# Optimization experiments

Hardware: AMD Instinct MI355X
Metric: run time of the kernel (lower is better)

## Reference

```python
import jax, jax.numpy as jnp
import numpy as np

N = 4096        # n_nodes; must equal HID due to the model's mean(dim=1)->classifier quirk
IN_DIM = 512
HID = 4096
E = 65536       # N * avg_degree(16)


def _lin(k, out_dim, in_dim):
    return jax.random.normal(k, (out_dim, in_dim), jnp.float32) * 0.02


def setup_inputs() -> dict:
    key = jax.random.key(0)
    ks = jax.random.split(key, 8)
    return {
        "x": jax.random.normal(ks[0], (N, IN_DIM), jnp.float32),
        "edge_index": jax.random.randint(ks[1], (2, E), 0, N, dtype=jnp.int32),
        "W_embed": _lin(ks[2], HID, IN_DIM),
        "b_embed": jnp.zeros((HID,), jnp.float32),
        "W1": _lin(ks[3], HID, HID),
        "b1": jnp.zeros((HID,), jnp.float32),
        "W2": _lin(ks[4], HID, HID),
        "b2": jnp.zeros((HID,), jnp.float32),
        "Wc1": _lin(ks[5], HID // 2, HID),
        "bc1": jnp.zeros((HID // 2,), jnp.float32),
        "Wc2": _lin(ks[6], 1, HID // 2),
        "bc2": jnp.zeros((1,), jnp.float32),
    }


def reference(x, edge_index, W_embed, b_embed, W1, b1, W2, b2, Wc1, bc1, Wc2, bc2):
    row, col = edge_index[0], edge_index[1]
    # embed: Linear(in_dim, hidden)
    h = x @ W_embed.T + b_embed                       # [N, HID]
    # two GNN layers: gather neighbors, scatter-add, linear + relu
    for W, b in ((W1, b1), (W2, b2)):
        aggr = jax.ops.segment_sum(h[col], row, num_segments=h.shape[0])  # [N, HID]
        h = jax.nn.relu(aggr @ W.T + b)
    # faithful to original: mean over feature dim -> [N] (N == HID)
    hm = jnp.mean(h, axis=1)                          # [HID]
    z = jax.nn.relu(hm @ Wc1.T + bc1)                 # [HID//2]
    out = (z @ Wc2.T + bc2).squeeze(-1)               # scalar
    return out
```

## Files before the change

### kernel.cpp

```cpp
#include <hip/hip_runtime.h>
#include <hip/hip_bf16.h>


#define N_NODES 4096
#define IN_DIM_ 512
#define HID_ 4096
#define NEDGE 65536

typedef float f32x4 __attribute__((ext_vector_type(4)));
typedef float f32x2 __attribute__((ext_vector_type(2)));
typedef unsigned short u16x8 __attribute__((ext_vector_type(8)));
typedef int i32x8 __attribute__((ext_vector_type(8)));

#define ACT_SCALE 8.0f
#define W_SCALE 256.0f
#define G_SCALE 8.0f
#define G_STORE_MUL (8.0f / 2048.0f)

__device__ __forceinline__ unsigned short f2bf(float f) {
  unsigned u = __float_as_uint(f);
  return (unsigned short)((u + 0x7fffu + ((u >> 16) & 1u)) >> 16);
}
__device__ __forceinline__ float bf2f(unsigned short h) {
  return __uint_as_float((unsigned)h << 16);
}
__device__ __forceinline__ unsigned char f2fp8(float f) {
  int w = __builtin_amdgcn_cvt_pk_fp8_f32(f, f, 0, false);
  return (unsigned char)(w & 0xff);
}
__device__ __forceinline__ void fp8x4_acc(int w, float* acc) {
  f32x2 lo = __builtin_amdgcn_cvt_pk_f32_fp8(w, false);
  f32x2 hi = __builtin_amdgcn_cvt_pk_f32_fp8(w, true);
  acc[0] += lo[0]; acc[1] += lo[1]; acc[2] += hi[0]; acc[3] += hi[1];
}

__global__ __launch_bounds__(256) void cvt_fp8(const float* __restrict__ in,
                                               unsigned char* __restrict__ out,
                                               int n, float scale) {
  int i = (blockIdx.x * 256 + threadIdx.x) * 8;
  if (i >= n) return;
  const float4 a = *(const float4*)(in + i);
  const float4 b = *(const float4*)(in + i + 4);
  int w0 = __builtin_amdgcn_cvt_pk_fp8_f32(a.x * scale, a.y * scale, 0, false);
  w0 = __builtin_amdgcn_cvt_pk_fp8_f32(a.z * scale, a.w * scale, w0, true);
  int w1 = __builtin_amdgcn_cvt_pk_fp8_f32(b.x * scale, b.y * scale, 0, false);
  w1 = __builtin_amdgcn_cvt_pk_fp8_f32(b.z * scale, b.w * scale, w1, true);
  *(int2*)(out + i) = make_int2(w0, w1);
}

__global__ __launch_bounds__(256) void zero_i32(int* __restrict__ p, int n) {
  int i = blockIdx.x * 256 + threadIdx.x;
  if (i < n) p[i] = 0;
}

__global__ __launch_bounds__(256) void hist_rows(const int* __restrict__ row,
                                                 int* __restrict__ counts) {
  int e = blockIdx.x * 256 + threadIdx.x;
  if (e < NEDGE) atomicAdd(&counts[row[e]], 1);
}

__global__ __launch_bounds__(1024) void scan4096(const int* __restrict__ counts,
                                                 int* __restrict__ starts) {
  __shared__ int sa[1024], sb[1024];
  const int t = threadIdx.x;
  const int c0 = counts[t * 4], c1 = counts[t * 4 + 1],
            c2 = counts[t * 4 + 2], c3 = counts[t * 4 + 3];
  const int local = c0 + c1 + c2 + c3;
  sa[t] = local;
  __syncthreads();
  int* src = sa; int* dst = sb;
  for (int off = 1; off < 1024; off <<= 1) {
    int v = src[t];
    if (t >= off) v += src[t - off];
    dst[t] = v;
    __syncthreads();
    int* tmp = src; src = dst; dst = tmp;
  }
  const int excl = (t == 0) ? 0 : src[t - 1];
  starts[t * 4]     = excl;
  starts[t * 4 + 1] = excl + c0;
  starts[t * 4 + 2] = excl + c0 + c1;
  starts[t * 4 + 3] = excl + c0 + c1 + c2;
  if (t == 1023) starts[4096] = excl + local;
}

__global__ __launch_bounds__(256) void fill_adj(const int* __restrict__ row,
                                                const int* __restrict__ col,
                                                const int* __restrict__ starts,
                                                int* __restrict__ cursor,
                                                int* __restrict__ adj) {
  int e = blockIdx.x * 256 + threadIdx.x;
  if (e >= NEDGE) return;
  int r = row[e];
  int p = atomicAdd(&cursor[r], 1);
  adj[starts[r] + p] = col[e];
}

__device__ __forceinline__ i32x8 ld_frag(const char* base0) {
  const int4 lo = *(const int4*)(base0);
  const int4 hi = *(const int4*)(base0 + 8192);
  i32x8 f;
  f[0] = lo.x; f[1] = lo.y; f[2] = lo.z; f[3] = lo.w;
  f[4] = hi.x; f[5] = hi.y; f[6] = hi.z; f[7] = hi.w;
  return f;
}

__global__ __launch_bounds__(256) void gemm_mx(
    const unsigned char* __restrict__ A, const unsigned char* __restrict__ B,
    unsigned char* __restrict__ C, int N, int K,
    const float* __restrict__ bias, float mul) {
  __shared__ unsigned char As[128 * 128];
  __shared__ unsigned char Bs[128 * 128];
  const int t = threadIdx.x;
  const int bm = blockIdx.x * 128, bn = blockIdx.y * 128;
  const int wave = t >> 6, lane = t & 63;
  const int wm = (wave >> 1) * 64, wn = (wave & 1) * 64;
  const int m16 = lane & 15, quad = lane >> 4;

  f32x4 acc[4][4] = {};

  const int srow = t >> 2;
  const int sg = (t & 3) * 32;
  const unsigned char* Ag0 = A + (size_t)(bm + srow) * K + sg;
  const unsigned char* Ag1 = A + (size_t)(bm + 64 + srow) * K + sg;
  const unsigned char* Bg0 = B + (size_t)(bn + srow) * K + sg;
  const unsigned char* Bg1 = B + (size_t)(bn + 64 + srow) * K + sg;
  char* AsB = (char*)As;
  char* BsB = (char*)Bs;

#define GLDS(gp, lp)                                                       \
  __builtin_amdgcn_global_load_lds(                                        \
      (const __attribute__((address_space(1))) void*)(gp),                 \
      (__attribute__((address_space(3))) void*)(lp), 16, 0, 0)

  for (int kb = 0; kb < K; kb += 128) {
    GLDS(Ag0 + kb,      AsB + t * 16);
    GLDS(Ag1 + kb,      AsB + 4096 + t * 16);
    GLDS(Ag0 + kb + 16, AsB + 8192 + t * 16);
    GLDS(Ag1 + kb + 16, AsB + 12288 + t * 16);
    GLDS(Bg0 + kb,      BsB + t * 16);
    GLDS(Bg1 + kb,      BsB + 4096 + t * 16);
    GLDS(Bg0 + kb + 16, BsB + 8192 + t * 16);
    GLDS(Bg1 + kb + 16, BsB + 12288 + t * 16);
    __syncthreads();

    i32x8 af[4], bfr[4];
#pragma unroll
    for (int r = 0; r < 4; ++r)
      af[r] = ld_frag(AsB + (wm + r * 16 + m16) * 64 + quad * 16);
#pragma unroll
    for (int c = 0; c < 4; ++c)
      bfr[c] = ld_frag(BsB + (wn + c * 16 + m16) * 64 + quad * 16);
#pragma unroll
    for (int r = 0; r < 4; ++r)
#pragma unroll
      for (int c = 0; c < 4; ++c)
        acc[r][c] = __builtin_amdgcn_mfma_scale_f32_16x16x128_f8f6f4(
            af[r], bfr[c], acc[r][c], 0, 0,
            0, 0x7f7f7f7f, 0, 0x7f7f7f7f);
    __syncthreads();
  }
#undef GLDS

#pragma unroll
  for (int r = 0; r < 4; ++r) {
#pragma unroll
    for (int c = 0; c < 4; ++c) {
      const int row0 = bm + wm + r * 16 + quad * 4;
      const int col = bn + wn + c * 16 + m16;
      const float bv = bias ? ACT_SCALE * bias[col] : 0.0f;
#pragma unroll
      for (int i = 0; i < 4; ++i) {
        C[(size_t)(row0 + i) * N + col] = f2fp8(acc[r][c][i] * mul + bv);
      }
    }
  }
}

__global__ __launch_bounds__(256) void aggr_f8out(
    const unsigned char* __restrict__ g, const int* __restrict__ starts,
    const int* __restrict__ adj, const float* __restrict__ bias,
    unsigned char* __restrict__ hout) {
  const int node = blockIdx.y;
  const int f0 = blockIdx.x * 2048 + threadIdx.x * 8;
  float acc[8] = {0, 0, 0, 0, 0, 0, 0, 0};
  const int s = starts[node], e = starts[node + 1];
  int j = s;
  for (; j + 4 <= e; j += 4) {
    const int c0 = adj[j], c1 = adj[j + 1], c2 = adj[j + 2], c3 = adj[j + 3];
    int2 v0 = *(const int2*)(g + (size_t)c0 * HID_ + f0);
    int2 v1 = *(const int2*)(g + (size_t)c1 * HID_ + f0);
    int2 v2 = *(const int2*)(g + (size_t)c2 * HID_ + f0);
    int2 v3 = *(const int2*)(g + (size_t)c3 * HID_ + f0);
    fp8x4_acc(v0.x, acc);     fp8x4_acc(v0.y, acc + 4);
    fp8x4_acc(v1.x, acc);     fp8x4_acc(v1.y, acc + 4);
    fp8x4_acc(v2.x, acc);     fp8x4_acc(v2.y, acc + 4);
    fp8x4_acc(v3.x, acc);     fp8x4_acc(v3.y, acc + 4);
  }
  for (; j < e; ++j) {
    int2 v = *(const int2*)(g + (size_t)adj[j] * HID_ + f0);
    fp8x4_acc(v.x, acc);      fp8x4_acc(v.y, acc + 4);
  }
  const float4 b0 = *(const float4*)(bias + f0);
  const float4 b1 = *(const float4*)(bias + f0 + 4);
  const float bb[8] = {b0.x, b0.y, b0.z, b0.w, b1.x, b1.y, b1.z, b1.w};
  float v[8];
#pragma unroll
  for (int i = 0; i < 8; ++i)
    v[i] = ACT_SCALE * fmaxf(acc[i] * (1.0f / G_SCALE) + bb[i], 0.0f);
  int w0 = __builtin_amdgcn_cvt_pk_fp8_f32(v[0], v[1], 0, false);
  w0 = __builtin_amdgcn_cvt_pk_fp8_f32(v[2], v[3], w0, true);
  int w1 = __builtin_amdgcn_cvt_pk_fp8_f32(v[4], v[5], 0, false);
  w1 = __builtin_amdgcn_cvt_pk_fp8_f32(v[6], v[7], w1, true);
  *(int2*)(hout + (size_t)node * HID_ + f0) = make_int2(w0, w1);
}

__global__ __launch_bounds__(256) void aggr_bf16out(
    const unsigned char* __restrict__ g, const int* __restrict__ starts,
    const int* __restrict__ adj, const float* __restrict__ bias,
    unsigned short* __restrict__ hout) {
  const int node = blockIdx.y;
  const int f0 = blockIdx.x * 2048 + threadIdx.x * 8;
  float acc[8] = {0, 0, 0, 0, 0, 0, 0, 0};
  const int s = starts[node], e = starts[node + 1];
  int j = s;
  for (; j + 4 <= e; j += 4) {
    const int c0 = adj[j], c1 = adj[j + 1], c2 = adj[j + 2], c3 = adj[j + 3];
    int2 v0 = *(const int2*)(g + (size_t)c0 * HID_ + f0);
    int2 v1 = *(const int2*)(g + (size_t)c1 * HID_ + f0);
    int2 v2 = *(const int2*)(g + (size_t)c2 * HID_ + f0);
    int2 v3 = *(const int2*)(g + (size_t)c3 * HID_ + f0);
    fp8x4_acc(v0.x, acc);     fp8x4_acc(v0.y, acc + 4);
    fp8x4_acc(v1.x, acc);     fp8x4_acc(v1.y, acc + 4);
    fp8x4_acc(v2.x, acc);     fp8x4_acc(v2.y, acc + 4);
    fp8x4_acc(v3.x, acc);     fp8x4_acc(v3.y, acc + 4);
  }
  for (; j < e; ++j) {
    int2 v = *(const int2*)(g + (size_t)adj[j] * HID_ + f0);
    fp8x4_acc(v.x, acc);      fp8x4_acc(v.y, acc + 4);
  }
  const float4 b0 = *(const float4*)(bias + f0);
  const float4 b1 = *(const float4*)(bias + f0 + 4);
  const float bb[8] = {b0.x, b0.y, b0.z, b0.w, b1.x, b1.y, b1.z, b1.w};
  u16x8 r;
#pragma unroll
  for (int i = 0; i < 8; ++i)
    r[i] = f2bf(fmaxf(acc[i] * (1.0f / G_SCALE) + bb[i], 0.0f));
  *(u16x8*)(hout + (size_t)node * HID_ + f0) = r;
}

__global__ __launch_bounds__(256) void row_mean(const unsigned short* __restrict__ h,
                                                float* __restrict__ hm) {
  const int row = blockIdx.x, t = threadIdx.x;
  const u16x8* p = (const u16x8*)(h + (size_t)row * HID_);
  u16x8 v1 = p[t], v2 = p[t + 256];
  float s = 0.f;
#pragma unroll
  for (int i = 0; i < 8; ++i) s += bf2f(v1[i]) + bf2f(v2[i]);
  for (int off = 32; off > 0; off >>= 1) s += __shfl_down(s, off);
  __shared__ float ws[4];
  if ((t & 63) == 0) ws[t >> 6] = s;
  __syncthreads();
  if (t == 0) hm[row] = (ws[0] + ws[1] + ws[2] + ws[3]) * (1.0f / (float)HID_);
}

__global__ __launch_bounds__(256) void clf1(const float* __restrict__ Wc1,
                                            const float* __restrict__ bc1,
                                            const float* __restrict__ hm,
                                            float* __restrict__ z) {
  const int wave = threadIdx.x >> 6, lane = threadIdx.x & 63;
  const int j = blockIdx.x * 4 + wave;
  const float* w = Wc1 + (size_t)j * HID_;
  float s = 0.f;
  for (int i = lane; i < HID_; i += 64) s += w[i] * hm[i];
  for (int off = 32; off > 0; off >>= 1) s += __shfl_down(s, off);
  if (lane == 0) z[j] = fmaxf(s + bc1[j], 0.0f);
}

__global__ __launch_bounds__(256) void clf2(const float* __restrict__ Wc2,
                                            const float* __restrict__ bc2,
                                            const float* __restrict__ z,
                                            float* __restrict__ out) {
  const int t = threadIdx.x;
  float s = 0.f;
  for (int i = t; i < HID_ / 2; i += 256) s += z[i] * Wc2[i];
  for (int off = 32; off > 0; off >>= 1) s += __shfl_down(s, off);
  __shared__ float ws[4];
  if ((t & 63) == 0) ws[t >> 6] = s;
  __syncthreads();
  if (t == 0) out[0] = ws[0] + ws[1] + ws[2] + ws[3] + bc2[0];
}

extern "C" void kernel_launch(void* const* d_in, const int* in_sizes, int n_in,
                              void* d_out, int out_size, void* d_ws, size_t ws_size,
                              hipStream_t stream) {
  (void)in_sizes; (void)n_in; (void)out_size; (void)ws_size;
  const float* x       = (const float*)d_in[0];
  const int*   edge    = (const int*)d_in[1];
  const int*   row     = edge;
  const int*   col     = edge + NEDGE;
  const float* W_embed = (const float*)d_in[2];
  const float* b_embed = (const float*)d_in[3];
  const float* W1      = (const float*)d_in[4];
  const float* b1      = (const float*)d_in[5];
  const float* W2      = (const float*)d_in[6];
  const float* b2      = (const float*)d_in[7];
  const float* Wc1     = (const float*)d_in[8];
  const float* bc1     = (const float*)d_in[9];
  const float* Wc2     = (const float*)d_in[10];
  const float* bc2     = (const float*)d_in[11];
  float* out = (float*)d_out;

  char* ws = (char*)d_ws;
  size_t off = 0;
  auto alloc = [&](size_t bytes) {
    char* p = ws + off;
    off += (bytes + 255) & ~(size_t)255;
    return p;
  };
  unsigned char*  xf8  = (unsigned char*)alloc((size_t)N_NODES * IN_DIM_);
  unsigned char*  wef8 = (unsigned char*)alloc((size_t)HID_ * IN_DIM_);
  unsigned char*  w1f8 = (unsigned char*)alloc((size_t)HID_ * HID_);
  unsigned char*  w2f8 = (unsigned char*)alloc((size_t)HID_ * HID_);
  unsigned char*  h0f8 = (unsigned char*)alloc((size_t)N_NODES * HID_);
  unsigned char*  h1f8 = (unsigned char*)alloc((size_t)N_NODES * HID_);
  unsigned char*  g    = (unsigned char*)alloc((size_t)N_NODES * HID_);
  unsigned short* h2   = (unsigned short*)alloc((size_t)N_NODES * HID_ * 2);
  int* counts = (int*)alloc(N_NODES * 4);
  int* cursor = (int*)alloc(N_NODES * 4);
  int* starts = (int*)alloc((N_NODES + 1) * 4);
  int* adj    = (int*)alloc(NEDGE * 4);
  float* hm   = (float*)alloc(N_NODES * 4);
  float* z    = (float*)alloc((HID_ / 2) * 4);

  zero_i32<<<16, 256, 0, stream>>>(counts, N_NODES);
  zero_i32<<<16, 256, 0, stream>>>(cursor, N_NODES);
  hist_rows<<<NEDGE / 256, 256, 0, stream>>>(row, counts);
  scan4096<<<1, 1024, 0, stream>>>(counts, starts);
  fill_adj<<<NEDGE / 256, 256, 0, stream>>>(row, col, starts, cursor, adj);

  cvt_fp8<<<(N_NODES * IN_DIM_ / 8) / 256, 256, 0, stream>>>(x, xf8, N_NODES * IN_DIM_, ACT_SCALE);
  cvt_fp8<<<(HID_ * IN_DIM_ / 8) / 256, 256, 0, stream>>>(W_embed, wef8, HID_ * IN_DIM_, W_SCALE);
  cvt_fp8<<<(HID_ * HID_ / 8) / 256, 256, 0, stream>>>(W1, w1f8, HID_ * HID_, W_SCALE);
  cvt_fp8<<<(HID_ * HID_ / 8) / 256, 256, 0, stream>>>(W2, w2f8, HID_ * HID_, W_SCALE);

  gemm_mx<<<dim3(32, 32), 256, 0, stream>>>(xf8, wef8, h0f8, HID_, IN_DIM_,
                                            b_embed, G_STORE_MUL);
  gemm_mx<<<dim3(32, 32), 256, 0, stream>>>(h0f8, w1f8, g, HID_, HID_,
                                            nullptr, G_STORE_MUL);
  aggr_f8out<<<dim3(2, N_NODES), 256, 0, stream>>>(g, starts, adj, b1, h1f8);
  gemm_mx<<<dim3(32, 32), 256, 0, stream>>>(h1f8, w2f8, g, HID_, HID_,
                                            nullptr, G_STORE_MUL);
  aggr_bf16out<<<dim3(2, N_NODES), 256, 0, stream>>>(g, starts, adj, b2, h2);
  row_mean<<<N_NODES, 256, 0, stream>>>(h2, hm);
  clf1<<<(HID_ / 2) / 4, 256, 0, stream>>>(Wc1, bc1, hm, z);
  clf2<<<1, 256, 0, stream>>>(Wc2, bc2, z, out);
}
```

Before: 483.6 us.

## Rewrite FP8 MX GEMM with 256x256 tiles, double-buffered LDS and swizzled layout

The MX-FP8 GEMM moves from 128x128 tiles with 4 waves to 256x256 tiles with 8 waves. It double-buffers 128 KB of LDS so the next K-tile's global-to-LDS loads overlap the current MFMAs. The LDS layout is XOR-swizzled to avoid bank conflicts, blocks are remapped onto the grid for L2 locality, and MFMA phases are interleaved with staged loads using setprio and barriers. This should raise arithmetic intensity and hide memory latency, at the cost of higher register and LDS use per block, which lowers occupancy.

Result: slower. 508.5 us (+5.2%).

```diff
diff --git a/kernel.cpp b/kernel.cpp
--- a/kernel.cpp
+++ b/kernel.cpp
@@ -96,74 +96,141 @@
   adj[starts[r] + p] = col[e];
 }
 
-__device__ __forceinline__ i32x8 ld_frag(const char* base0) {
-  const int4 lo = *(const int4*)(base0);
-  const int4 hi = *(const int4*)(base0 + 8192);
-  i32x8 f;
-  f[0] = lo.x; f[1] = lo.y; f[2] = lo.z; f[3] = lo.w;
-  f[4] = hi.x; f[5] = hi.y; f[6] = hi.z; f[7] = hi.w;
-  return f;
-}
-
-__global__ __launch_bounds__(256) void gemm_mx(
-    const unsigned char* __restrict__ A, const unsigned char* __restrict__ B,
-    unsigned char* __restrict__ C, int N, int K,
-    const float* __restrict__ bias, float mul) {
-  __shared__ unsigned char As[128 * 128];
-  __shared__ unsigned char Bs[128 * 128];
-  const int t = threadIdx.x;
-  const int bm = blockIdx.x * 128, bn = blockIdx.y * 128;
-  const int wave = t >> 6, lane = t & 63;
-  const int wm = (wave >> 1) * 64, wn = (wave & 1) * 64;
-  const int m16 = lane & 15, quad = lane >> 4;
-
-  f32x4 acc[4][4] = {};
-
-  const int srow = t >> 2;
-  const int sg = (t & 3) * 32;
-  const unsigned char* Ag0 = A + (size_t)(bm + srow) * K + sg;
-  const unsigned char* Ag1 = A + (size_t)(bm + 64 + srow) * K + sg;
-  const unsigned char* Bg0 = B + (size_t)(bn + srow) * K + sg;
-  const unsigned char* Bg1 = B + (size_t)(bn + 64 + srow) * K + sg;
-  char* AsB = (char*)As;
-  char* BsB = (char*)Bs;
-
 #define GLDS(gp, lp)                                                       \
   __builtin_amdgcn_global_load_lds(                                        \
       (const __attribute__((address_space(1))) void*)(gp),                 \
       (__attribute__((address_space(3))) void*)(lp), 16, 0, 0)
 
-  for (int kb = 0; kb < K; kb += 128) {
-    GLDS(Ag0 + kb,      AsB + t * 16);
-    GLDS(Ag1 + kb,      AsB + 4096 + t * 16);
-    GLDS(Ag0 + kb + 16, AsB + 8192 + t * 16);
-    GLDS(Ag1 + kb + 16, AsB + 12288 + t * 16);
-    GLDS(Bg0 + kb,      BsB + t * 16);
-    GLDS(Bg1 + kb,      BsB + 4096 + t * 16);
-    GLDS(Bg0 + kb + 16, BsB + 8192 + t * 16);
-    GLDS(Bg1 + kb + 16, BsB + 12288 + t * 16);
-    __syncthreads();
-
-    i32x8 af[4], bfr[4];
-#pragma unroll
-    for (int r = 0; r < 4; ++r)
-      af[r] = ld_frag(AsB + (wm + r * 16 + m16) * 64 + quad * 16);
-#pragma unroll
-    for (int c = 0; c < 4; ++c)
-      bfr[c] = ld_frag(BsB + (wn + c * 16 + m16) * 64 + quad * 16);
-#pragma unroll
-    for (int r = 0; r < 4; ++r)
-#pragma unroll
-      for (int c = 0; c < 4; ++c)
-        acc[r][c] = __builtin_amdgcn_mfma_scale_f32_16x16x128_f8f6f4(
-            af[r], bfr[c], acc[r][c], 0, 0,
-            0, 0x7f7f7f7f, 0, 0x7f7f7f7f);
-    __syncthreads();
-  }
-#undef GLDS
-
-#pragma unroll
-  for (int r = 0; r < 4; ++r) {
+__global__ __launch_bounds__(512, 2) void gemm_mx(
+    const unsigned char* __restrict__ A, const unsigned char* __restrict__ B,
+    unsigned char* __restrict__ C, int N, int K,
+    const float* __restrict__ bias, float mul) {
+  __shared__ unsigned char lds[131072];
+  const int t = threadIdx.x;
+  const int w = blockIdx.x;
+  const int L = (w & 7) * 32 + (w >> 3);
+  const int bm = (L & 15) * 256, bn = (L >> 4) * 256;
+  const int wave = t >> 6, lane = t & 63;
+  const int wm = (wave >> 2) * 128, wn = (wave & 3) * 64;
+  const int m16 = lane & 15, quad = lane >> 4;
+
+  f32x4 acc[8][4] = {};
+
+  const int rS = t >> 3;
+  const int sS = ((t & 7) ^ (rS & 7)) << 4;
+  const unsigned char* Ag = A + (size_t)(bm + rS) * K + sS;
+  const unsigned char* Bg = B + (size_t)(bn + rS) * K + sS;
+  const size_t rstep = (size_t)64 * K;
+  unsigned char* Als = lds;
+  unsigned char* Bls = lds + 65536;
+  const int sd = t * 16;
+
+  const int o0 = ((quad << 1) ^ (lane & 7)) << 4;
+  const int o1 = o0 ^ 16;
+
+  const int KT = K >> 7;
+
+#define STAGE_A(i, kb, dst) GLDS(Ag + (kb) + (size_t)(i) * rstep, (dst) + (i) * 8192 + sd)
+#define STAGE_B(i, kb, dst) GLDS(Bg + (kb) + (size_t)(i) * rstep, (dst) + (i) * 8192 + sd)
+
+#define LDFRAG(dst, base, row)                                             \
+  {                                                                        \
+    const unsigned char* _p = (base) + (row) * 128;                        \
+    const int4 _lo = *(const int4*)(_p + o0);                              \
+    const int4 _hi = *(const int4*)(_p + o1);                              \
+    dst[0] = _lo.x; dst[1] = _lo.y; dst[2] = _lo.z; dst[3] = _lo.w;        \
+    dst[4] = _hi.x; dst[5] = _hi.y; dst[6] = _hi.z; dst[7] = _hi.w;        \
+  }
+
+#define MFMA(r, c, afr, bfr)                                               \
+  acc[r][c] = __builtin_amdgcn_mfma_scale_f32_16x16x128_f8f6f4(            \
+      afr, bfr, acc[r][c], 0, 0, 0, 0x7f7f7f7f, 0, 0x7f7f7f7f)
+
+  STAGE_A(0, 0, Als); STAGE_A(1, 0, Als); STAGE_A(2, 0, Als); STAGE_A(3, 0, Als);
+  STAGE_B(0, 0, Bls); STAGE_B(1, 0, Bls); STAGE_B(2, 0, Bls); STAGE_B(3, 0, Bls);
+  asm volatile("s_waitcnt vmcnt(0)" ::: "memory");
+  __builtin_amdgcn_s_barrier();
+
+  i32x8 af[4], bf01[2], bf23[2];
+
+  for (int tt = 0; tt < KT; ++tt) {
+    unsigned char* Ab = Als + (tt & 1) * 32768;
+    unsigned char* Bb = Bls + (tt & 1) * 32768;
+    unsigned char* An = Als + ((tt + 1) & 1) * 32768;
+    unsigned char* Bn = Bls + ((tt + 1) & 1) * 32768;
+    const int kbn = (tt + 1) << 7;
+    const bool more = (tt + 1) < KT;
+
+    LDFRAG(af[0], Ab, wm + m16);
+    LDFRAG(af[1], Ab, wm + 16 + m16);
+    LDFRAG(af[2], Ab, wm + 32 + m16);
+    LDFRAG(af[3], Ab, wm + 48 + m16);
+    LDFRAG(bf01[0], Bb, wn + m16);
+    LDFRAG(bf01[1], Bb, wn + 16 + m16);
+    if (more) { STAGE_A(0, kbn, An); STAGE_A(1, kbn, An); }
+    __builtin_amdgcn_s_barrier();
+    asm volatile("s_waitcnt lgkmcnt(0)" ::: "memory");
+    __builtin_amdgcn_sched_barrier(0);
+    __builtin_amdgcn_s_setprio(1);
+    MFMA(0, 0, af[0], bf01[0]); MFMA(0, 1, af[0], bf01[1]);
+    MFMA(1, 0, af[1], bf01[0]); MFMA(1, 1, af[1], bf01[1]);
+    MFMA(2, 0, af[2], bf01[0]); MFMA(2, 1, af[2], bf01[1]);
+    MFMA(3, 0, af[3], bf01[0]); MFMA(3, 1, af[3], bf01[1]);
+    __builtin_amdgcn_s_setprio(0);
+    __builtin_amdgcn_s_barrier();
+
+    LDFRAG(bf23[0], Bb, wn + 32 + m16);
+    LDFRAG(bf23[1], Bb, wn + 48 + m16);
+    if (more) { STAGE_A(2, kbn, An); STAGE_A(3, kbn, An); }
+    __builtin_amdgcn_s_barrier();
+    asm volatile("s_waitcnt lgkmcnt(0)" ::: "memory");
+    __builtin_amdgcn_sched_barrier(0);
+    __builtin_amdgcn_s_setprio(1);
+    MFMA(0, 2, af[0], bf23[0]); MFMA(0, 3, af[0], bf23[1]);
+    MFMA(1, 2, af[1], bf23[0]); MFMA(1, 3, af[1], bf23[1]);
+    MFMA(2, 2, af[2], bf23[0]); MFMA(2, 3, af[2], bf23[1]);
+    MFMA(3, 2, af[3], bf23[0]); MFMA(3, 3, af[3], bf23[1]);
+    __builtin_amdgcn_s_setprio(0);
+    __builtin_amdgcn_s_barrier();
+
+    LDFRAG(af[0], Ab, wm + 64 + m16);
+    LDFRAG(af[1], Ab, wm + 80 + m16);
+    LDFRAG(af[2], Ab, wm + 96 + m16);
+    LDFRAG(af[3], Ab, wm + 112 + m16);
+    if (more) { STAGE_B(0, kbn, Bn); STAGE_B(1, kbn, Bn); }
+    __builtin_amdgcn_s_barrier();
+    asm volatile("s_waitcnt lgkmcnt(0)" ::: "memory");
+    __builtin_amdgcn_sched_barrier(0);
+    __builtin_amdgcn_s_setprio(1);
+    MFMA(4, 0, af[0], bf01[0]); MFMA(4, 1, af[0], bf01[1]);
+    MFMA(5, 0, af[1], bf01[0]); MFMA(5, 1, af[1], bf01[1]);
+    MFMA(6, 0, af[2], bf01[0]); MFMA(6, 1, af[2], bf01[1]);
+    MFMA(7, 0, af[3], bf01[0]); MFMA(7, 1, af[3], bf01[1]);
+    __builtin_amdgcn_s_setprio(0);
+    __builtin_amdgcn_s_barrier();
+
+    if (more) { STAGE_B(2, kbn, Bn); STAGE_B(3, kbn, Bn); }
+    __builtin_amdgcn_s_barrier();
+    __builtin_amdgcn_s_setprio(1);
+    MFMA(4, 2, af[0], bf23[0]); MFMA(4, 3, af[0], bf23[1]);
+    MFMA(5, 2, af[1], bf23[0]); MFMA(5, 3, af[1], bf23[1]);
+    MFMA(6, 2, af[2], bf23[0]); MFMA(6, 3, af[2], bf23[1]);
+    MFMA(7, 2, af[3], bf23[0]); MFMA(7, 3, af[3], bf23[1]);
+    __builtin_amdgcn_s_setprio(0);
+    if (more) {
+      asm volatile("s_waitcnt vmcnt(0)" ::: "memory");
+      __builtin_amdgcn_sched_barrier(0);
+    }
+    __builtin_amdgcn_s_barrier();
+  }
+
+#undef MFMA
+#undef LDFRAG
+#undef STAGE_A
+#undef STAGE_B
+
+#pragma unroll
+  for (int r = 0; r < 8; ++r) {
 #pragma unroll
     for (int c = 0; c < 4; ++c) {
       const int row0 = bm + wm + r * 16 + quad * 4;
@@ -176,6 +243,7 @@
     }
   }
 }
+#undef GLDS
 
 __global__ __launch_bounds__(256) void aggr_f8out(
     const unsigned char* __restrict__ g, const int* __restrict__ starts,
@@ -344,13 +412,13 @@
   cvt_fp8<<<(HID_ * HID_ / 8) / 256, 256, 0, stream>>>(W1, w1f8, HID_ * HID_, W_SCALE);
   cvt_fp8<<<(HID_ * HID_ / 8) / 256, 256, 0, stream>>>(W2, w2f8, HID_ * HID_, W_SCALE);
 
-  gemm_mx<<<dim3(32, 32), 256, 0, stream>>>(xf8, wef8, h0f8, HID_, IN_DIM_,
-                                            b_embed, G_STORE_MUL);
-  gemm_mx<<<dim3(32, 32), 256, 0, stream>>>(h0f8, w1f8, g, HID_, HID_,
-                                            nullptr, G_STORE_MUL);
+  gemm_mx<<<256, 512, 0, stream>>>(xf8, wef8, h0f8, HID_, IN_DIM_,
+                                   b_embed, G_STORE_MUL);
+  gemm_mx<<<256, 512, 0, stream>>>(h0f8, w1f8, g, HID_, HID_,
+                                   nullptr, G_STORE_MUL);
   aggr_f8out<<<dim3(2, N_NODES), 256, 0, stream>>>(g, starts, adj, b1, h1f8);
-  gemm_mx<<<dim3(32, 32), 256, 0, stream>>>(h1f8, w2f8, g, HID_, HID_,
-                                            nullptr, G_STORE_MUL);
+  gemm_mx<<<256, 512, 0, stream>>>(h1f8, w2f8, g, HID_, HID_,
+                                   nullptr, G_STORE_MUL);
   aggr_bf16out<<<dim3(2, N_NODES), 256, 0, stream>>>(g, starts, adj, b2, h2);
   row_mean<<<N_NODES, 256, 0, stream>>>(h2, hm);
   clf1<<<(HID_ / 2) / 4, 256, 0, stream>>>(Wc1, bc1, hm, z);
```
